# Kernel optimization log

Measured on AMD Instinct MI355X. Metric: run time of the kernel, lower is better.

## Reference

```python
import jax, jax.numpy as jnp
import numpy as np

KERNEL_LIST = (4, 8)
STRIDE = 4
EXT = 1
NUM_HEADS = 4
KEY_DIM = 32   # head_dim * attn_ratio = 64 * 0.5
HEAD_DIM = 64
SCALE = KEY_DIM ** -0.5


def _pool_matrix(inp, out):
    # torch adaptive_avg_pool2d: window i covers [floor(i*inp/out), ceil((i+1)*inp/out))
    P = np.zeros((out, inp), np.float32)
    for i in range(out):
        s0 = (i * inp) // out
        e0 = -((-(i + 1) * inp) // out)
        P[i, s0:e0] = 1.0 / (e0 - s0)
    return jnp.asarray(P)


def _dwconv3(x, w, b):
    # depthwise 3x3 conv, padding 1 (groups == channels)
    y = jax.lax.conv_general_dilated(
        x, w, window_strides=(1, 1), padding=((1, 1), (1, 1)),
        feature_group_count=x.shape[1],
        dimension_numbers=("NCHW", "OIHW", "NCHW"))
    return y + b[None, :, None, None]


def _attention(x, qkv_w, qkv_b, proj_w, proj_b, pe_w, pe_b):
    B, C, H, W = x.shape
    N = H * W
    qkv = jnp.einsum("oc,bchw->bohw", qkv_w, x) + qkv_b[None, :, None, None]
    qkv = qkv.reshape(B, NUM_HEADS, 2 * KEY_DIM + HEAD_DIM, N)
    q = qkv[:, :, :KEY_DIM]                # (B,h,kd,N)
    k = qkv[:, :, KEY_DIM:2 * KEY_DIM]     # (B,h,kd,N)
    v = qkv[:, :, 2 * KEY_DIM:]            # (B,h,hd,N)
    attn = jax.nn.softmax(jnp.einsum("bhkn,bhkm->bhnm", q, k) * SCALE, axis=-1)
    # v @ attn^T : out[d,n] = sum_m v[d,m] * attn[n,m]
    o = jnp.einsum("bhdm,bhnm->bhdn", v, attn).reshape(B, C, H, W)
    o = o + _dwconv3(v.reshape(B, C, H, W), pe_w, pe_b)
    return jnp.einsum("oc,bchw->bohw", proj_w, o) + proj_b[None, :, None, None]


def _extract(xp, Kp, s):
    # overlapping patches; layout (N, C, Lh, Kp, Lw, Kp); window order is (lh, lw)
    N, C, Hp, Wp = xp.shape
    Lh = (Hp - Kp) // s + 1
    Lw = (Wp - Kp) // s + 1
    hi = jnp.arange(Lh)[:, None] * s + jnp.arange(Kp)[None, :]  # (Lh, Kp)
    wi = jnp.arange(Lw)[:, None] * s + jnp.arange(Kp)[None, :]
    p = xp[:, :, hi, :]          # (N, C, Lh, Kp, Wp)
    p = p[:, :, :, :, wi]        # (N, C, Lh, Kp, Lw, Kp)
    return p, Lh, Lw


def setup_inputs() -> dict:
    key = jax.random.key(0)
    ks = jax.random.split(key, 9)
    C = 256
    w = 0.02
    return {
        "x": jax.random.normal(ks[0], (8, C, 64, 64), jnp.float32),
        "qkv_w": jax.random.normal(ks[1], (512, C), jnp.float32) * w,
        "qkv_b": jax.random.normal(ks[2], (512,), jnp.float32) * w,
        "proj_w": jax.random.normal(ks[3], (C, C), jnp.float32) * w,
        "proj_b": jax.random.normal(ks[4], (C,), jnp.float32) * w,
        "attn_pe_w": jax.random.normal(ks[5], (C, 1, 3, 3), jnp.float32) * w,
        "attn_pe_b": jax.random.normal(ks[6], (C,), jnp.float32) * w,
        "dp_pe_w": jax.random.normal(ks[7], (C, 1, 3, 3), jnp.float32) * w,
        "dp_pe_b": jax.random.normal(ks[8], (C,), jnp.float32) * w,
    }


def reference(x, qkv_w, qkv_b, proj_w, proj_b, attn_pe_w, attn_pe_b, dp_pe_w, dp_pe_b):
    N, C, H, W = x.shape
    xp = jnp.pad(x, ((0, 0), (0, 0), (EXT, EXT), (EXT, EXT)), mode="edge")  # replicate pad
    outs = [x]
    for K in KERNEL_LIST:
        Kp = K + 2 * EXT
        p, Lh, Lw = _extract(xp, Kp, STRIDE)
        P = _pool_matrix(Kp, K)
        # adaptive avg pool Kp->K on both spatial dims; windows ordered (lh, lw)
        pooled = jnp.einsum("pi,ncaibj,qj->nabcpq", P, p, P)
        pooled = pooled.reshape(N * Lh * Lw, C, K, K)
        y = _dwconv3(pooled, dp_pe_w, dp_pe_b) + pooled
        a = _attention(y, qkv_w, qkv_b, proj_w, proj_b, attn_pe_w, attn_pe_b)
        # torch does a raw .view(N, C*K*K, L) on the (N*L, C, K, K) buffer
        cols = a.reshape(N, C, K, K, Lh, Lw)
        cols_p = cols.transpose(0, 1, 2, 4, 3, 5)  # (N, C, K, Lh, K, Lw)
        hh = jnp.arange(Lh)[None, :] * STRIDE + jnp.arange(K)[:, None]  # (K, Lh)
        ww = jnp.arange(Lw)[None, :] * STRIDE + jnp.arange(K)[:, None]  # (K, Lw)
        folded = jnp.zeros((N, C, H, W), x.dtype).at[
            :, :, hh[:, :, None, None], ww[None, None, :, :]].add(cols_p)
        count = jnp.zeros((1, 1, H, W), x.dtype).at[
            :, :, hh[:, :, None, None], ww[None, None, :, :]].add(
            jnp.ones((1, 1, K, Lh, K, Lw), x.dtype))
        outs.append(folded / count)
    return sum(outs) / len(outs)
```

## Files before the change

kernel.cpp:

```cpp
#include <hip/hip_runtime.h>
#include <hip/hip_bf16.h>

typedef __bf16 bf16x8 __attribute__((ext_vector_type(8)));
typedef float  f32x4  __attribute__((ext_vector_type(4)));

#define DEV static __device__ __forceinline__

DEV float bf2f(ushort u) { unsigned x = ((unsigned)u) << 16; return __uint_as_float(x); }
DEV ushort f2bf(float f) {
    unsigned u = __float_as_uint(f);
    unsigned r = (u + 0x7FFFu + ((u >> 16) & 1u)) >> 16;
    return (ushort)r;
}

typedef __attribute__((address_space(1))) const unsigned int gu32;
typedef __attribute__((address_space(3))) unsigned int lu32;
DEV void gload16(const ushort* g, ushort* l) {
    __builtin_amdgcn_global_load_lds((gu32*)g, (lu32*)l, 16, 0, 0);
}

__global__ __launch_bounds__(256) void f2bf_kernel(
    const float* __restrict__ src, ushort* __restrict__ dst)
{
    int i = (blockIdx.x * 256 + threadIdx.x) * 4;
    float4 v = *(const float4*)(src + i);
    ushort4 o;
    o.x = f2bf(v.x); o.y = f2bf(v.y); o.z = f2bf(v.z); o.w = f2bf(v.w);
    *(ushort4*)(dst + i) = o;
}

__global__ __launch_bounds__(256) void pe_prep_kernel(
    const float* __restrict__ apw, ushort* __restrict__ wt)
{
    int i = blockIdx.x * 256 + threadIdx.x;
    if (i < 9 * 256) {
        int tap = i >> 8, c = i & 255;
        wt[i] = f2bf(apw[c * 9 + tap]);
    }
}

__global__ __launch_bounds__(256) void box_kernel(
    const float* __restrict__ x,
    ushort* __restrict__ B)
{
    int br = blockIdx.x % 65; int g = blockIdx.x / 65;
    const float* xg = x + (size_t)g * 256 * 4096;
    ushort* Bg = B + (size_t)g * 65 * 65 * 256;
    const int r0 = max(br - 1, 0) * 64;
    const int r1 = min(br, 63) * 64;
    __shared__ float s[128][65];
    const int wl = threadIdx.x & 63, cq = threadIdx.x >> 6;
    const int c2 = threadIdx.x & 127, bh = threadIdx.x >> 7;
    for (int half = 0; half < 2; ++half) {
#pragma unroll 4
        for (int it = 0; it < 32; ++it) {
            int cl_ = it * 4 + cq;
            const float* xp = xg + (size_t)(half * 128 + cl_) * 4096;
            s[cl_][wl] = xp[r0 + wl] + xp[r1 + wl];
        }
        __syncthreads();
        for (int bc = bh; bc < 65; bc += 2) {
            float v = 0.25f * (s[c2][max(bc - 1, 0)] + s[c2][min(bc, 63)]);
            Bg[((size_t)br * 65 + bc) * 256 + half * 128 + c2] = f2bf(v);
        }
        __syncthreads();
    }
}

template<int K, int L>
__global__ __launch_bounds__(256) void pool_kernel(
    const ushort* __restrict__ B,
    const float* __restrict__ w9,
    const float* __restrict__ bias,
    ushort* __restrict__ y)
{
    constexpr int HF = K / 2;
    const int pk = blockIdx.x;
    const int lw = pk % L; int t = pk / L; const int lh = t % L; const int g = t / L;
    const int c = threadIdx.x;
    const ushort* Bg = B + (size_t)g * 65 * 65 * 256 + c;
    float pool[K][K];
#pragma unroll
    for (int p = 0; p < K; ++p) {
        const int br = lh * 4 + p + (p >= HF ? 1 : 0);
#pragma unroll
        for (int q = 0; q < K; ++q) {
            const int bc = lw * 4 + q + (q >= HF ? 1 : 0);
            pool[p][q] = bf2f(Bg[((size_t)br * 65 + bc) * 256]);
        }
    }
    float wv[9];
#pragma unroll
    for (int i = 0; i < 9; ++i) wv[i] = w9[c * 9 + i];
    const float bv = bias[c];
    ushort* yp = y + (size_t)pk * (K * K) * 256 + c;
#pragma unroll
    for (int p = 0; p < K; ++p) {
#pragma unroll
        for (int q = 0; q < K; ++q) {
            float a = pool[p][q] + bv;
#pragma unroll
            for (int dp = -1; dp <= 1; ++dp) {
#pragma unroll
                for (int dq = -1; dq <= 1; ++dq) {
                    int pp = p + dp, qq = q + dq;
                    if (pp >= 0 && pp < K && qq >= 0 && qq < K)
                        a += wv[(dp + 1) * 3 + (dq + 1)] * pool[pp][qq];
                }
            }
            yp[(p * K + q) * 256] = f2bf(a);
        }
    }
}

template<int OC, int EPI, int K, int L, int RT>
__global__ __launch_bounds__(256) void gemm_kernel(
    const ushort* __restrict__ act,
    const ushort* __restrict__ w,
    const float* __restrict__ bias,
    ushort* __restrict__ out_bf)
{
    __shared__ __attribute__((aligned(16))) ushort As[128][32];
    __shared__ __attribute__((aligned(16))) ushort Ws[128][32];
    constexpr int NT = OC / 128;
    const int id  = blockIdx.x;
    const int xc  = id & 7;
    const int ctb = (id >> 3) % NT;
    const int tt  = id / (8 * NT);
    const int rowt = tt * 8 + xc;
    if (rowt >= RT) return;
    const int tid  = threadIdx.x;
    const int n0   = rowt * 128;
    const int ch0  = ctb * 128;
    const int wv   = tid >> 6, lane = tid & 63;
    const int l15  = lane & 15, quad = lane >> 4;
    const int wm   = wv >> 1, wn = wv & 1;

    const int qlog = (lane & 3) ^ ((lane >> 3) & 3);
    const size_t soff = (size_t)(lane >> 2) * 256 + (size_t)qlog * 8;
    const ushort* aS0 = act + ((size_t)n0 + wv * 32) * 256 + soff;
    const ushort* wS0 = w   + ((size_t)ch0 + wv * 32) * 256 + soff;
    const ushort* aS1 = aS0 + 16 * 256;
    const ushort* wS1 = wS0 + 16 * 256;
    ushort* aD0 = &As[wv * 32][0];
    ushort* wD0 = &Ws[wv * 32][0];
    ushort* aD1 = aD0 + 16 * 32;
    ushort* wD1 = wD0 + 16 * 32;

    const int rcol = (quad ^ ((l15 >> 1) & 3)) * 8;
    f32x4 acc[4][4] = {};
    for (int k0 = 0; k0 < 256; k0 += 32) {
        gload16(aS0 + k0, aD0);
        gload16(aS1 + k0, aD1);
        gload16(wS0 + k0, wD0);
        gload16(wS1 + k0, wD1);
        __syncthreads();
        bf16x8 af[4], bw[4];
#pragma unroll
        for (int t = 0; t < 4; ++t) {
            af[t] = *(const bf16x8*)&As[wm * 64 + t * 16 + l15][rcol];
            bw[t] = *(const bf16x8*)&Ws[wn * 64 + t * 16 + l15][rcol];
        }
#pragma unroll
        for (int mt = 0; mt < 4; ++mt)
#pragma unroll
            for (int nt = 0; nt < 4; ++nt)
                acc[mt][nt] = __builtin_amdgcn_mfma_f32_16x16x32_bf16(af[mt], bw[nt], acc[mt][nt], 0, 0, 0);
        __syncthreads();
    }

    float bv[4];
#pragma unroll
    for (int nt = 0; nt < 4; ++nt) bv[nt] = bias[ch0 + wn * 64 + nt * 16 + l15];
#pragma unroll
    for (int mt = 0; mt < 4; ++mt) {
#pragma unroll
        for (int r = 0; r < 4; ++r) {
            const int n = n0 + wm * 64 + mt * 16 + quad * 4 + r;
            if (EPI == 0) {
                ushort* dst = out_bf + (size_t)n * OC + ch0 + wn * 64;
#pragma unroll
                for (int nt = 0; nt < 4; ++nt)
                    dst[nt * 16 + l15] = f2bf(acc[mt][nt][r] + bv[nt]);
            } else {
                constexpr int K2 = K * K;
                constexpr int LL = L * L;
                const int b_g   = n >> (K == 8 ? 6 : 4);
                const int pq    = n & (K2 - 1);
                const int gl    = b_g / LL;
                const int b_loc = b_g - gl * LL;
                const size_t base = (size_t)gl * (256 * K2 * LL) + (size_t)b_loc * 256 * K2 + pq;
#pragma unroll
                for (int nt = 0; nt < 4; ++nt) {
                    const int ch = ch0 + wn * 64 + nt * 16 + l15;
                    out_bf[base + (size_t)ch * K2] = f2bf(acc[mt][nt][r] + bv[nt]);
                }
            }
        }
    }
}

__global__ __launch_bounds__(128) void attn8_mfma_kernel(
    const ushort* __restrict__ qkv,
    const ushort* __restrict__ wt,
    const float* __restrict__ pe_b,
    ushort* __restrict__ o_out)
{
    constexpr float SCALE = 0.17677669529663687f;
    __shared__ __attribute__((aligned(16))) ushort Pl[64][72];
    __shared__ __attribute__((aligned(16))) ushort Vt[64][72];
    __shared__ __attribute__((aligned(16))) ushort Vr[64][72];
    __shared__ __attribute__((aligned(16))) ushort wsh[9][64];
    __shared__ float bsh[64];
    const int tid  = threadIdx.x;
    const int lane = tid & 63;
    const int ww   = tid >> 6;
    const int b    = blockIdx.x >> 2;
    const int h    = blockIdx.x & 3;
    const int cbase = h * 64;
    const int l15  = lane & 15, quad = lane >> 4;
    const ushort* base = qkv + (size_t)b * 64 * 512 + h * 128;

    if (tid < 72) {
        int tap = tid / 8, cl8 = (tid & 7) * 8;
        *(uint4*)&wsh[tap][cl8] = *(const uint4*)&wt[tap * 256 + cbase + cl8];
    }
    if (tid < 64) bsh[tid] = pe_b[cbase + tid];

    {
        const int m = lane;
        const ushort* vsrc = base + (size_t)m * 512 + 64 + ww * 32;
        const int d0 = ww * 32;
#pragma unroll
        for (int t = 0; t < 4; ++t) {
            uint4 vv = *(const uint4*)(vsrc + t * 8);
            *(uint4*)&Vr[m][d0 + t * 8] = vv;
            unsigned u[4] = {vv.x, vv.y, vv.z, vv.w};
#pragma unroll
            for (int e = 0; e < 4; ++e) {
                Vt[d0 + t * 8 + e * 2][m]     = (ushort)(u[e] & 0xFFFF);
                Vt[d0 + t * 8 + e * 2 + 1][m] = (ushort)(u[e] >> 16);
            }
        }
    }

    bf16x8 fq[2];
#pragma unroll
    for (int s = 0; s < 2; ++s) {
        int n = (ww + 2 * s) * 16 + l15;
        fq[s] = *(const bf16x8*)(base + (size_t)n * 512 + quad * 8);
    }
    f32x4 S[2][4];
#pragma unroll
    for (int mt = 0; mt < 4; ++mt) {
        int m = mt * 16 + l15;
        bf16x8 fk = *(const bf16x8*)(base + (size_t)m * 512 + 32 + quad * 8);
#pragma unroll
        for (int s = 0; s < 2; ++s) {
            f32x4 z = {0.f, 0.f, 0.f, 0.f};
            S[s][mt] = __builtin_amdgcn_mfma_f32_16x16x32_bf16(fq[s], fk, z, 0, 0, 0);
        }
    }
    __syncthreads();

    {
        const int d8  = (tid & 7) * 8;
        const int nb  = tid >> 3;
        float pe[4][8];
#pragma unroll
        for (int e = 0; e < 8; ++e) {
            float pb = bsh[d8 + e];
#pragma unroll
            for (int it = 0; it < 4; ++it) pe[it][e] = pb;
        }
#pragma unroll
        for (int tap = 0; tap < 9; ++tap) {
            const int dp = tap / 3 - 1, dq = tap % 3 - 1;
            uint4 wv4 = *(const uint4*)&wsh[tap][d8];
            unsigned uw[4] = {wv4.x, wv4.y, wv4.z, wv4.w};
            float wlo[4], whi[4];
#pragma unroll
            for (int e2 = 0; e2 < 4; ++e2) {
                wlo[e2] = __uint_as_float(uw[e2] << 16);
                whi[e2] = __uint_as_float(uw[e2] & 0xFFFF0000u);
            }
#pragma unroll
            for (int it = 0; it < 4; ++it) {
                const int n = nb + 16 * it;
                const int pp = (n >> 3) + dp, qq = (n & 7) + dq;
                if (pp >= 0 && pp < 8 && qq >= 0 && qq < 8) {
                    uint4 vv = *(const uint4*)&Vr[pp * 8 + qq][d8];
                    unsigned uv[4] = {vv.x, vv.y, vv.z, vv.w};
#pragma unroll
                    for (int e2 = 0; e2 < 4; ++e2) {
                        float vlo = __uint_as_float(uv[e2] << 16);
                        float vhi = __uint_as_float(uv[e2] & 0xFFFF0000u);
                        pe[it][2 * e2]     += wlo[e2] * vlo;
                        pe[it][2 * e2 + 1] += whi[e2] * vhi;
                    }
                }
            }
        }
#pragma unroll
        for (int it = 0; it < 4; ++it) {
            const int n = nb + 16 * it;
            ushort pk[8];
#pragma unroll
            for (int e = 0; e < 8; ++e) pk[e] = f2bf(pe[it][e]);
            *(uint4*)&Pl[n][d8] = *(const uint4*)pk;
        }
    }
    __syncthreads();

    f32x4 O[2][4];
#pragma unroll
    for (int s = 0; s < 2; ++s)
#pragma unroll
        for (int dt = 0; dt < 4; ++dt)
#pragma unroll
            for (int r = 0; r < 4; ++r)
                O[s][dt][r] = bf2f(Pl[(ww + 2 * s) * 16 + quad * 4 + r][dt * 16 + l15]);

#pragma unroll
    for (int s = 0; s < 2; ++s) {
#pragma unroll
        for (int r = 0; r < 4; ++r) {
            float mx = -1e30f;
#pragma unroll
            for (int mt = 0; mt < 4; ++mt) { S[s][mt][r] *= SCALE; mx = fmaxf(mx, S[s][mt][r]); }
            mx = fmaxf(mx, __shfl_xor(mx, 1));
            mx = fmaxf(mx, __shfl_xor(mx, 2));
            mx = fmaxf(mx, __shfl_xor(mx, 4));
            mx = fmaxf(mx, __shfl_xor(mx, 8));
            float sum = 0.f;
#pragma unroll
            for (int mt = 0; mt < 4; ++mt) { float e = __expf(S[s][mt][r] - mx); S[s][mt][r] = e; sum += e; }
            sum += __shfl_xor(sum, 1);
            sum += __shfl_xor(sum, 2);
            sum += __shfl_xor(sum, 4);
            sum += __shfl_xor(sum, 8);
            float inv = 1.f / sum;
#pragma unroll
            for (int mt = 0; mt < 4; ++mt) S[s][mt][r] *= inv;
        }
    }
    __syncthreads();

#pragma unroll
    for (int s = 0; s < 2; ++s)
#pragma unroll
        for (int r = 0; r < 4; ++r) {
            int n = (ww + 2 * s) * 16 + quad * 4 + r;
#pragma unroll
            for (int mt = 0; mt < 4; ++mt)
                Pl[n][mt * 16 + l15] = f2bf(S[s][mt][r]);
        }
    __syncthreads();

#pragma unroll
    for (int ks = 0; ks < 2; ++ks) {
        bf16x8 fp[2], fv[4];
#pragma unroll
        for (int s = 0; s < 2; ++s)
            fp[s] = *(const bf16x8*)&Pl[(ww + 2 * s) * 16 + l15][ks * 32 + quad * 8];
#pragma unroll
        for (int dt = 0; dt < 4; ++dt)
            fv[dt] = *(const bf16x8*)&Vt[dt * 16 + l15][ks * 32 + quad * 8];
#pragma unroll
        for (int s = 0; s < 2; ++s)
#pragma unroll
            for (int dt = 0; dt < 4; ++dt)
                O[s][dt] = __builtin_amdgcn_mfma_f32_16x16x32_bf16(fp[s], fv[dt], O[s][dt], 0, 0, 0);
    }

#pragma unroll
    for (int s = 0; s < 2; ++s) {
#pragma unroll
        for (int r = 0; r < 4; ++r) {
            int n = (ww + 2 * s) * 16 + quad * 4 + r;
#pragma unroll
            for (int dt = 0; dt < 4; ++dt)
                Pl[n][dt * 16 + l15] = f2bf(O[s][dt][r]);
        }
    }
    __syncthreads();

#pragma unroll
    for (int it = 0; it < 4; ++it) {
        int cidx = it * 128 + tid;
        int row = cidx >> 3, c8 = (cidx & 7) * 8;
        uint4 v = *(const uint4*)&Pl[row][c8];
        *(uint4*)(o_out + (size_t)(b * 64 + row) * 256 + cbase + c8) = v;
    }
}

__global__ __launch_bounds__(256) void attn4_mfma_kernel(
    const ushort* __restrict__ qkv,
    const ushort* __restrict__ wt,
    const float* __restrict__ pe_b,
    ushort* __restrict__ o_out)
{
    constexpr float SCALE = 0.17677669529663687f;
    __shared__ __attribute__((aligned(16))) ushort wsh[9][256];
    __shared__ float bsh[256];
    __shared__ __attribute__((aligned(16))) ushort Vt4[4][64][32];
    __shared__ __attribute__((aligned(16))) ushort VP[4][16][64];
    __shared__ __attribute__((aligned(16))) ushort Pm[4][16][32];
    const int tid  = threadIdx.x;
    const int lane = tid & 63;
    const int w    = tid >> 6;
    const int b    = blockIdx.x;
    const int h    = w;
    const int cbase = h * 64;
    const int l15  = lane & 15, quad = lane >> 4;
    const ushort* base = qkv + (size_t)b * 16 * 512 + h * 128;

    for (int i = tid; i < 9 * 32; i += 256) {
        int tap = i >> 5, c8 = (i & 31) * 8;
        *(uint4*)&wsh[tap][c8] = *(const uint4*)&wt[tap * 256 + c8];
    }
    bsh[tid] = pe_b[tid];
    __syncthreads();

    {
        uint4 z = {0u, 0u, 0u, 0u};
#pragma unroll
        for (int t = 0; t < 4; ++t)
            *(uint4*)&Vt4[w][t * 16 + (lane >> 2)][(lane & 3) * 8] = z;
        *(uint4*)&Pm[w][lane >> 2][(lane & 3) * 8] = z;
    }

    {
        const int m = lane & 15, dblk = lane >> 4;
        const ushort* vsrc = base + (size_t)m * 512 + 64 + dblk * 16;
        uint4 v0 = *(const uint4*)(vsrc);
        uint4 v1 = *(const uint4*)(vsrc + 8);
        *(uint4*)&VP[w][m][dblk * 16]     = v0;
        *(uint4*)&VP[w][m][dblk * 16 + 8] = v1;
        ushort us[16];
        *(uint4*)&us[0] = v0; *(uint4*)&us[8] = v1;
        const int mb = m >> 3, m7 = m & 7;
#pragma unroll
        for (int e = 0; e < 16; ++e) {
            int d = dblk * 16 + e;
            Vt4[w][d][((mb ^ (d & 3)) << 3) + m7] = us[e];
        }
    }

    bf16x8 fq = *(const bf16x8*)(base + (size_t)l15 * 512 + quad * 8);
    bf16x8 fk = *(const bf16x8*)(base + (size_t)l15 * 512 + 32 + quad * 8);
    f32x4 z4 = {0.f, 0.f, 0.f, 0.f};
    f32x4 S = __builtin_amdgcn_mfma_f32_16x16x32_bf16(fq, fk, z4, 0, 0, 0);

    float p[4];
#pragma unroll
    for (int r = 0; r < 4; ++r) {
        float v = S[r] * SCALE;
        float mx = v;
        mx = fmaxf(mx, __shfl_xor(mx, 1));
        mx = fmaxf(mx, __shfl_xor(mx, 2));
        mx = fmaxf(mx, __shfl_xor(mx, 4));
        mx = fmaxf(mx, __shfl_xor(mx, 8));
        float e = __expf(v - mx);
        float sum = e;
        sum += __shfl_xor(sum, 1);
        sum += __shfl_xor(sum, 2);
        sum += __shfl_xor(sum, 4);
        sum += __shfl_xor(sum, 8);
        p[r] = e / sum;
    }
#pragma unroll
    for (int r = 0; r < 4; ++r) {
        int n = quad * 4 + r;
        Pm[w][n][(((l15 >> 3) ^ (n & 3)) << 3) + (l15 & 7)] = f2bf(p[r]);
    }

    float pe[2][8];
    const int n_ = lane & 15;
    const int pp0 = n_ >> 2, qq0 = n_ & 3;
#pragma unroll
    for (int it = 0; it < 2; ++it) {
        int ch = (lane >> 4) + it * 4;
#pragma unroll
        for (int e = 0; e < 8; ++e) pe[it][e] = bsh[cbase + ch * 8 + e];
    }
#pragma unroll
    for (int tap = 0; tap < 9; ++tap) {
        const int dp = tap / 3 - 1, dq = tap % 3 - 1;
        const int pp = pp0 + dp, qq = qq0 + dq;
        if (pp >= 0 && pp < 4 && qq >= 0 && qq < 4) {
            const int mm = pp * 4 + qq;
#pragma unroll
            for (int it = 0; it < 2; ++it) {
                int ch = (lane >> 4) + it * 4;
                uint4 wv4 = *(const uint4*)&wsh[tap][cbase + ch * 8];
                uint4 vv  = *(const uint4*)&VP[w][mm][ch * 8];
                unsigned uw[4] = {wv4.x, wv4.y, wv4.z, wv4.w};
                unsigned uv[4] = {vv.x, vv.y, vv.z, vv.w};
#pragma unroll
                for (int e2 = 0; e2 < 4; ++e2) {
                    float wlo = __uint_as_float(uw[e2] << 16);
                    float whi = __uint_as_float(uw[e2] & 0xFFFF0000u);
                    float vlo = __uint_as_float(uv[e2] << 16);
                    float vhi = __uint_as_float(uv[e2] & 0xFFFF0000u);
                    pe[it][2 * e2]     += wlo * vlo;
                    pe[it][2 * e2 + 1] += whi * vhi;
                }
            }
        }
    }
#pragma unroll
    for (int it = 0; it < 2; ++it) {
        int ch = (lane >> 4) + it * 4;
        ushort pk[8];
#pragma unroll
        for (int e = 0; e < 8; ++e) pk[e] = f2bf(pe[it][e]);
        *(uint4*)&VP[w][n_][ch * 8] = *(const uint4*)pk;
    }

    f32x4 O[4];
#pragma unroll
    for (int dt = 0; dt < 4; ++dt)
#pragma unroll
        for (int r = 0; r < 4; ++r)
            O[dt][r] = bf2f(VP[w][quad * 4 + r][dt * 16 + l15]);

    bf16x8 fp = *(const bf16x8*)&Pm[w][l15][((quad ^ (l15 & 3)) << 3)];
#pragma unroll
    for (int dt = 0; dt < 4; ++dt) {
        bf16x8 fv = *(const bf16x8*)&Vt4[w][dt * 16 + l15][((quad ^ (l15 & 3)) << 3)];
        O[dt] = __builtin_amdgcn_mfma_f32_16x16x32_bf16(fp, fv, O[dt], 0, 0, 0);
    }

#pragma unroll
    for (int dt = 0; dt < 4; ++dt)
#pragma unroll
        for (int r = 0; r < 4; ++r)
            VP[w][quad * 4 + r][dt * 16 + l15] = f2bf(O[dt][r]);

#pragma unroll
    for (int j = 0; j < 2; ++j) {
        int idx = j * 64 + lane;
        int row = idx >> 3, c8 = (idx & 7) * 8;
        uint4 v = *(const uint4*)&VP[w][row][c8];
        *(uint4*)(o_out + (size_t)(b * 16 + row) * 256 + cbase + c8) = v;
    }
}

__global__ __launch_bounds__(256) void final_kernel(
    const float* __restrict__ x,
    const ushort* __restrict__ s8,
    const ushort* __restrict__ s4,
    float* __restrict__ out)
{
    const int c2 = blockIdx.x & 255;
    const int g  = blockIdx.x >> 8;
    const ushort* s8g = s8 + (size_t)g * (256 * 64 * 225);
    const ushort* s4g = s4 + (size_t)g * (256 * 16 * 256);
    const float third = 1.f / 3.f;
#pragma unroll 2
    for (int it = 0; it < 16; ++it) {
        int pix = it * 256 + threadIdx.x;
        int h = pix >> 6, w = pix & 63;
        int f4 = ((((c2 * 4 + (h & 3)) * 4 + (w & 3)) * 16 + (h >> 2)) * 16) + (w >> 2);
        float v4 = bf2f(s4g[f4]);
        int lh_lo = (h >= 8) ? ((h - 4) >> 2) : 0, lh_hi = min(14, h >> 2);
        int lw_lo = (w >= 8) ? ((w - 4) >> 2) : 0, lw_hi = min(14, w >> 2);
        float v8 = 0.f;
        for (int lh2 = lh_lo; lh2 <= lh_hi; ++lh2) {
            int p2 = h - lh2 * 4;
            for (int lw2 = lw_lo; lw2 <= lw_hi; ++lw2) {
                int q2 = w - lw2 * 4;
                int f8 = (((c2 * 8 + p2) * 8 + q2) * 15 + lh2) * 15 + lw2;
                v8 += bf2f(s8g[f8]);
            }
        }
        float inv = 1.f / (float)((lh_hi - lh_lo + 1) * (lw_hi - lw_lo + 1));
        size_t off = ((size_t)(g * 256 + c2)) * 4096 + pix;
        out[off] = (x[off] + v8 * inv + v4) * third;
    }
}

extern "C" void kernel_launch(void* const* d_in, const int* in_sizes, int n_in,
                              void* d_out, int out_size, void* d_ws, size_t ws_size,
                              hipStream_t stream)
{
    const float* x      = (const float*)d_in[0];
    const float* qkv_w  = (const float*)d_in[1];
    const float* qkv_b  = (const float*)d_in[2];
    const float* proj_w = (const float*)d_in[3];
    const float* proj_b = (const float*)d_in[4];
    const float* apw    = (const float*)d_in[5];
    const float* apb    = (const float*)d_in[6];
    const float* dpw    = (const float*)d_in[7];
    const float* dpb    = (const float*)d_in[8];
    float* out = (float*)d_out;

    const size_t S8_B = 8ull * 225 * 256 * 64 * 2;
    const size_t S4_B = 8ull * 256 * 256 * 16 * 2;
    const size_t Y_B  = 4ull * 14400 * 256 * 2;
    const size_t Q_B  = 4ull * 14400 * 512 * 2;
    const size_t W_B  = (512ull * 256 + 256ull * 256 + 9ull * 256) * 2;
    const size_t B_B  = 8ull * 65 * 65 * 256 * 2;
    if (ws_size < S8_B + S4_B + Y_B + Q_B + W_B + B_B) {
        hipMemsetAsync(d_out, 0x46, 4, stream);
        return;
    }
    ushort* s8    = (ushort*)d_ws;
    ushort* s4    = s8 + S8_B / 2;
    ushort* ybuf  = s4 + S4_B / 2;
    ushort* qbuf  = ybuf + Y_B / 2;
    ushort* qw_bf = qbuf + Q_B / 2;
    ushort* pw_bf = qw_bf + 512 * 256;
    ushort* wt    = pw_bf + 256 * 256;
    ushort* Bbuf  = (ushort*)((char*)d_ws + S8_B + S4_B + Y_B + Q_B + W_B);

    f2bf_kernel<<<128, 256, 0, stream>>>(qkv_w, qw_bf);
    f2bf_kernel<<<64, 256, 0, stream>>>(proj_w, pw_bf);
    pe_prep_kernel<<<9, 256, 0, stream>>>(apw, wt);
    box_kernel<<<8 * 65, 256, 0, stream>>>(x, Bbuf);

    for (int hf = 0; hf < 2; ++hf) {
        ushort* B_h = Bbuf + (size_t)hf * 4 * 65 * 65 * 256;
        ushort* s8_h = s8 + (size_t)hf * 4 * 225 * 256 * 64;
        pool_kernel<8, 15><<<4 * 225, 256, 0, stream>>>(B_h, dpw, dpb, ybuf);
        gemm_kernel<512, 0, 8, 15, 450><<<57 * 8 * 4, 256, 0, stream>>>(ybuf, qw_bf, qkv_b, qbuf);
        attn8_mfma_kernel<<<900 * 4, 128, 0, stream>>>(qbuf, wt, apb, ybuf);
        gemm_kernel<256, 1, 8, 15, 450><<<57 * 8 * 2, 256, 0, stream>>>(ybuf, pw_bf, proj_b, s8_h);
    }
    pool_kernel<4, 16><<<8 * 256, 256, 0, stream>>>(Bbuf, dpw, dpb, ybuf);
    gemm_kernel<512, 0, 4, 16, 256><<<32 * 8 * 4, 256, 0, stream>>>(ybuf, qw_bf, qkv_b, qbuf);
    attn4_mfma_kernel<<<2048, 256, 0, stream>>>(qbuf, wt, apb, ybuf);
    gemm_kernel<256, 1, 4, 16, 256><<<32 * 8 * 2, 256, 0, stream>>>(ybuf, pw_bf, proj_b, s4);

    final_kernel<<<2048, 256, 0, stream>>>(x, s8, s4, out);
}
```

Measured before the change: 383.8 us.

## Restructure attn8 kernel to drop Vr buffer and most block barriers

The 8x8 attention kernel no longer keeps a separate row-major V copy in LDS. The depthwise positional-encoding conv now reads the transposed V tile, with one thread per channel handling whole rows of 8 using register-held weights. Each wave loads only its own half of the weights and bias and writes and reads back only its own rows of the shared P/O buffer, so three of the block barriers are removed and a min-occupancy hint is added to launch bounds. This lowers LDS use and synchronisation, but correctness now depends on each wave's accesses staying confined to its own rows and channels.

```diff
diff --git a/kernel.cpp b/kernel.cpp
--- a/kernel.cpp
+++ b/kernel.cpp
@@ -200,16 +200,15 @@
     }
 }
 
-__global__ __launch_bounds__(128) void attn8_mfma_kernel(
+__global__ __launch_bounds__(128, 4) void attn8_mfma_kernel(
     const ushort* __restrict__ qkv,
     const ushort* __restrict__ wt,
     const float* __restrict__ pe_b,
     ushort* __restrict__ o_out)
 {
     constexpr float SCALE = 0.17677669529663687f;
-    __shared__ __attribute__((aligned(16))) ushort Pl[64][72];
+    __shared__ __attribute__((aligned(16))) ushort PB[64][72];
     __shared__ __attribute__((aligned(16))) ushort Vt[64][72];
-    __shared__ __attribute__((aligned(16))) ushort Vr[64][72];
     __shared__ __attribute__((aligned(16))) ushort wsh[9][64];
     __shared__ float bsh[64];
     const int tid  = threadIdx.x;
@@ -221,11 +220,11 @@
     const int l15  = lane & 15, quad = lane >> 4;
     const ushort* base = qkv + (size_t)b * 64 * 512 + h * 128;
 
-    if (tid < 72) {
-        int tap = tid / 8, cl8 = (tid & 7) * 8;
-        *(uint4*)&wsh[tap][cl8] = *(const uint4*)&wt[tap * 256 + cbase + cl8];
-    }
-    if (tid < 64) bsh[tid] = pe_b[cbase + tid];
+    if (lane < 36) {
+        int tap = lane >> 2, c8 = (lane & 3) * 8;
+        *(uint4*)&wsh[tap][ww * 32 + c8] = *(const uint4*)&wt[tap * 256 + cbase + ww * 32 + c8];
+    }
+    if (lane < 32) bsh[ww * 32 + lane] = pe_b[cbase + ww * 32 + lane];
 
     {
         const int m = lane;
@@ -234,7 +233,6 @@
 #pragma unroll
         for (int t = 0; t < 4; ++t) {
             uint4 vv = *(const uint4*)(vsrc + t * 8);
-            *(uint4*)&Vr[m][d0 + t * 8] = vv;
             unsigned u[4] = {vv.x, vv.y, vv.z, vv.w};
 #pragma unroll
             for (int e = 0; e < 4; ++e) {
@@ -261,53 +259,39 @@
             S[s][mt] = __builtin_amdgcn_mfma_f32_16x16x32_bf16(fq[s], fk, z, 0, 0, 0);
         }
     }
-    __syncthreads();
 
     {
-        const int d8  = (tid & 7) * 8;
-        const int nb  = tid >> 3;
-        float pe[4][8];
-#pragma unroll
-        for (int e = 0; e < 8; ++e) {
-            float pb = bsh[d8 + e];
-#pragma unroll
-            for (int it = 0; it < 4; ++it) pe[it][e] = pb;
-        }
-#pragma unroll
-        for (int tap = 0; tap < 9; ++tap) {
-            const int dp = tap / 3 - 1, dq = tap % 3 - 1;
-            uint4 wv4 = *(const uint4*)&wsh[tap][d8];
-            unsigned uw[4] = {wv4.x, wv4.y, wv4.z, wv4.w};
-            float wlo[4], whi[4];
-#pragma unroll
-            for (int e2 = 0; e2 < 4; ++e2) {
-                wlo[e2] = __uint_as_float(uw[e2] << 16);
-                whi[e2] = __uint_as_float(uw[e2] & 0xFFFF0000u);
-            }
-#pragma unroll
-            for (int it = 0; it < 4; ++it) {
-                const int n = nb + 16 * it;
-                const int pp = (n >> 3) + dp, qq = (n & 7) + dq;
-                if (pp >= 0 && pp < 8 && qq >= 0 && qq < 8) {
-                    uint4 vv = *(const uint4*)&Vr[pp * 8 + qq][d8];
-                    unsigned uv[4] = {vv.x, vv.y, vv.z, vv.w};
-#pragma unroll
-                    for (int e2 = 0; e2 < 4; ++e2) {
-                        float vlo = __uint_as_float(uv[e2] << 16);
-                        float vhi = __uint_as_float(uv[e2] & 0xFFFF0000u);
-                        pe[it][2 * e2]     += wlo[e2] * vlo;
-                        pe[it][2 * e2 + 1] += whi[e2] * vhi;
-                    }
+        const int d   = ww * 32 + (lane & 31);
+        const int pb4 = (lane >> 5) * 4;
+        float wreg[9];
+#pragma unroll
+        for (int i = 0; i < 9; ++i) wreg[i] = bf2f(wsh[i][d]);
+        const float bias0 = bsh[d];
+#pragma unroll
+        for (int it = 0; it < 4; ++it) {
+            const int p = pb4 + it;
+            float pe[8];
+#pragma unroll
+            for (int q = 0; q < 8; ++q) pe[q] = bias0;
+#pragma unroll
+            for (int dpi = 0; dpi < 3; ++dpi) {
+                const int pp = p + dpi - 1;
+                if (pp >= 0 && pp < 8) {
+                    bf16x8 v8 = *(const bf16x8*)&Vt[d][pp * 8];
+                    float v[8];
+#pragma unroll
+                    for (int e = 0; e < 8; ++e) v[e] = (float)v8[e];
+                    const float w0 = wreg[dpi * 3], w1 = wreg[dpi * 3 + 1], w2 = wreg[dpi * 3 + 2];
+                    pe[0] += w1 * v[0] + w2 * v[1];
+#pragma unroll
+                    for (int q = 1; q < 7; ++q) pe[q] += w0 * v[q - 1] + w1 * v[q] + w2 * v[q + 1];
+                    pe[7] += w0 * v[6] + w1 * v[7];
                 }
             }
-        }
-#pragma unroll
-        for (int it = 0; it < 4; ++it) {
-            const int n = nb + 16 * it;
             ushort pk[8];
 #pragma unroll
-            for (int e = 0; e < 8; ++e) pk[e] = f2bf(pe[it][e]);
-            *(uint4*)&Pl[n][d8] = *(const uint4*)pk;
+            for (int e = 0; e < 8; ++e) pk[e] = f2bf(pe[e]);
+            *(uint4*)&PB[d][p * 8] = *(const uint4*)pk;
         }
     }
     __syncthreads();
@@ -316,10 +300,13 @@
 #pragma unroll
     for (int s = 0; s < 2; ++s)
 #pragma unroll
-        for (int dt = 0; dt < 4; ++dt)
-#pragma unroll
-            for (int r = 0; r < 4; ++r)
-                O[s][dt][r] = bf2f(Pl[(ww + 2 * s) * 16 + quad * 4 + r][dt * 16 + l15]);
+        for (int dt = 0; dt < 4; ++dt) {
+            ushort4 t4 = *(const ushort4*)&PB[dt * 16 + l15][(ww + 2 * s) * 16 + quad * 4];
+            O[s][dt][0] = bf2f(t4.x);
+            O[s][dt][1] = bf2f(t4.y);
+            O[s][dt][2] = bf2f(t4.z);
+            O[s][dt][3] = bf2f(t4.w);
+        }
 
 #pragma unroll
     for (int s = 0; s < 2; ++s) {
@@ -353,16 +340,15 @@
             int n = (ww + 2 * s) * 16 + quad * 4 + r;
 #pragma unroll
             for (int mt = 0; mt < 4; ++mt)
-                Pl[n][mt * 16 + l15] = f2bf(S[s][mt][r]);
-        }
-    __syncthreads();
+                PB[n][mt * 16 + l15] = f2bf(S[s][mt][r]);
+        }
 
 #pragma unroll
     for (int ks = 0; ks < 2; ++ks) {
         bf16x8 fp[2], fv[4];
 #pragma unroll
         for (int s = 0; s < 2; ++s)
-            fp[s] = *(const bf16x8*)&Pl[(ww + 2 * s) * 16 + l15][ks * 32 + quad * 8];
+            fp[s] = *(const bf16x8*)&PB[(ww + 2 * s) * 16 + l15][ks * 32 + quad * 8];
 #pragma unroll
         for (int dt = 0; dt < 4; ++dt)
             fv[dt] = *(const bf16x8*)&Vt[dt * 16 + l15][ks * 32 + quad * 8];
@@ -374,22 +360,20 @@
     }
 
 #pragma unroll
-    for (int s = 0; s < 2; ++s) {
+    for (int s = 0; s < 2; ++s)
 #pragma unroll
         for (int r = 0; r < 4; ++r) {
             int n = (ww + 2 * s) * 16 + quad * 4 + r;
 #pragma unroll
             for (int dt = 0; dt < 4; ++dt)
-                Pl[n][dt * 16 + l15] = f2bf(O[s][dt][r]);
-        }
-    }
-    __syncthreads();
-
+                PB[n][dt * 16 + l15] = f2bf(O[s][dt][r]);
+        }
 #pragma unroll
     for (int it = 0; it < 4; ++it) {
-        int cidx = it * 128 + tid;
-        int row = cidx >> 3, c8 = (cidx & 7) * 8;
-        uint4 v = *(const uint4*)&Pl[row][c8];
+        int cidx = it * 64 + lane;
+        int rl = cidx >> 3, c8 = (cidx & 7) * 8;
+        int row = ww * 16 + (rl & 15) + (rl >> 4) * 32;
+        uint4 v = *(const uint4*)&PB[row][c8];
         *(uint4*)(o_out + (size_t)(b * 64 + row) * 256 + cbase + c8) = v;
     }
 }
```

Result: no change. 390.7 us (+1.8%).
